# Performance work log

Hardware: AMD Instinct MI355X
Metric: run time of the kernel (lower is better)

The kernel has to match this reference:

```python
import jax, jax.numpy as jnp
import numpy as np
from jax import lax

BN_EPS = 1e-5
DN = ('NCHW', 'OIHW', 'NCHW')


def _bn_silu(y, s, b, m, v):
    # eval-mode BatchNorm2d followed by SiLU
    inv = s / jnp.sqrt(v + BN_EPS)
    y = y * inv[None, :, None, None] + (b - m * inv)[None, :, None, None]
    return jax.nn.silu(y)


def _dsconv(x, dw_w, pw_w, s, b, m, v):
    c = x.shape[1]
    y = lax.conv_general_dilated(x, dw_w, (1, 1), [(1, 1), (1, 1)],
                                 dimension_numbers=DN, feature_group_count=c)
    y = lax.conv_general_dilated(y, pw_w, (1, 1), [(0, 0), (0, 0)],
                                 dimension_numbers=DN)
    return _bn_silu(y, s, b, m, v)


def setup_inputs() -> dict:
    key = jax.random.key(0)
    ks = jax.random.split(key, 8)
    B, C, H, W, OUT, TOPK = 32, 256, 64, 64, 256, 2
    CS = C // 2
    inp = {
        'x': jax.random.normal(ks[0], (B, C, H, W), jnp.float32),
        'weights': jax.random.uniform(ks[1], (B, TOPK), jnp.float32),
        'indices': jax.random.randint(ks[2], (B, TOPK), 0, 4),
        'dw_w0': jax.random.normal(ks[3], (CS, 1, 3, 3), jnp.float32) * 0.1,
        'pw_w0': jax.random.normal(ks[4], (OUT, CS, 1, 1), jnp.float32) * 0.05,
        'bn0_s': jnp.ones((OUT,), jnp.float32),
        'bn0_b': jnp.zeros((OUT,), jnp.float32),
        'bn0_m': jnp.zeros((OUT,), jnp.float32),
        'bn0_v': jnp.ones((OUT,), jnp.float32),
        'dw_w1': jax.random.normal(ks[5], (CS, 1, 3, 3), jnp.float32) * 0.1,
        'pw_w1': jax.random.normal(ks[6], (OUT, CS, 1, 1), jnp.float32) * 0.05,
        'bn1_s': jnp.ones((OUT,), jnp.float32),
        'bn1_b': jnp.zeros((OUT,), jnp.float32),
        'bn1_m': jnp.zeros((OUT,), jnp.float32),
        'bn1_v': jnp.ones((OUT,), jnp.float32),
        'w2': jax.random.normal(ks[7], (OUT, C, 1, 1), jnp.float32) * 0.05,
        'bn2_s': jnp.ones((OUT,), jnp.float32),
        'bn2_b': jnp.zeros((OUT,), jnp.float32),
        'bn2_m': jnp.zeros((OUT,), jnp.float32),
        'bn2_v': jnp.ones((OUT,), jnp.float32),
    }
    return inp


def reference(x, weights, indices,
              dw_w0, pw_w0, bn0_s, bn0_b, bn0_m, bn0_v,
              dw_w1, pw_w1, bn1_s, bn1_b, bn1_m, bn1_v,
              w2, bn2_s, bn2_b, bn2_m, bn2_v):
    cs = x.shape[1] // 2
    x_rgb, x_ir = x[:, :cs], x[:, cs:]
    # Per-expert routing coefficient: sum over top-k slots of weight * (index == e).
    # Mathematically identical to the torch masked scatter-add loop.
    def coeff(e):
        return jnp.sum(weights * (indices == e).astype(weights.dtype), axis=1)  # [B]
    e0 = _dsconv(x_rgb, dw_w0, pw_w0, bn0_s, bn0_b, bn0_m, bn0_v)
    e1 = _dsconv(x_ir, dw_w1, pw_w1, bn1_s, bn1_b, bn1_m, bn1_v)
    e2 = _bn_silu(lax.conv_general_dilated(x, w2, (1, 1), [(0, 0), (0, 0)],
                                           dimension_numbers=DN),
                  bn2_s, bn2_b, bn2_m, bn2_v)
    out = (coeff(0)[:, None, None, None] * e0
           + coeff(1)[:, None, None, None] * e1
           + coeff(2)[:, None, None, None] * e2)
    return out
```

## Files before the change

kernel.cpp:

```cpp
#include <hip/hip_runtime.h>

typedef __bf16 bf16x8 __attribute__((ext_vector_type(8)));
typedef float f32x4 __attribute__((ext_vector_type(4)));

#define BN_EPS 1e-5f

__device__ __forceinline__ unsigned short f2bf(float f) {
    union { float f; unsigned u; } x; x.f = f;
    unsigned r = x.u + 0x7fffu + ((x.u >> 16) & 1u);
    return (unsigned short)(r >> 16);
}

__device__ __forceinline__ unsigned pk_bf16(float lo, float hi) {
    unsigned r;
    asm("v_cvt_pk_bf16_f32 %0, %1, %2" : "=v"(r) : "v"(lo), "v"(hi));
    return r;
}

__device__ __forceinline__ float fcomp(float4 v, int j) {
    return (j == 0) ? v.x : (j == 1) ? v.y : (j == 2) ? v.z : v.w;
}

__global__ void prep_kernel(const float* __restrict__ pw0, const float* __restrict__ pw1,
                            const float* __restrict__ w2,
                            const float* __restrict__ s0, const float* __restrict__ b0,
                            const float* __restrict__ m0, const float* __restrict__ v0,
                            const float* __restrict__ s1, const float* __restrict__ b1,
                            const float* __restrict__ m1, const float* __restrict__ v1,
                            const float* __restrict__ s2, const float* __restrict__ b2,
                            const float* __restrict__ m2, const float* __restrict__ v2,
                            unsigned short* __restrict__ wfF0, unsigned short* __restrict__ wfF1,
                            unsigned short* __restrict__ wfF2, float* __restrict__ beta) {
    int o = blockIdx.x;
    int t = threadIdx.x;
    float inv0 = s0[o] * rsqrtf(v0[o] + BN_EPS);
    float inv1 = s1[o] * rsqrtf(v1[o] + BN_EPS);
    float inv2 = s2[o] * rsqrtf(v2[o] + BN_EPS);
    if (t == 0) {
        beta[0 * 256 + o] = b0[o] - m0[o] * inv0;
        beta[1 * 256 + o] = b1[o] - m1[o] * inv1;
        beta[2 * 256 + o] = b2[o] - m2[o] * inv2;
    }
    if (t < 128) {
        wfF0[((t >> 3) * 256 + o) * 8 + (t & 7)] = f2bf(pw0[o * 128 + t] * inv0);
        wfF1[((t >> 3) * 256 + o) * 8 + (t & 7)] = f2bf(pw1[o * 128 + t] * inv1);
    }
    wfF2[((t >> 3) * 256 + o) * 8 + (t & 7)] = f2bf(w2[o * 256 + t] * inv2);
}

__device__ __forceinline__ void loadA0(const unsigned short* __restrict__ W,
                                       int wave, int l15, int l4, bf16x8 a[2]) {
    const int row0 = wave * 32 + l15;
    a[0] = *(const bf16x8*)(W + (l4 * 256 + row0) * 8);
    a[1] = *(const bf16x8*)(W + (l4 * 256 + row0 + 16) * 8);
}

template<int NK>
__device__ __forceinline__ void gemm_expert(const char* lds, const unsigned short* __restrict__ W,
                                            int qb, int wave, int l15, int l4,
                                            const int* pxv, const int* swv,
                                            const bf16x8 aPre[2], f32x4 acc[2][4]) {
    const int row0 = wave * 32 + l15;
    bf16x8 aC[2], bC[4];
    aC[0] = aPre[0]; aC[1] = aPre[1];
#pragma unroll
    for (int tp = 0; tp < 4; ++tp)
        bC[tp] = *(const bf16x8*)(lds + pxv[tp] * 512 + ((qb + l4 * 16) ^ swv[tp]));

#pragma unroll
    for (int kk = 0; kk < NK; ++kk) {
        bf16x8 aN[2], bN[4];
        if (kk + 1 < NK) {
#pragma unroll
            for (int ot = 0; ot < 2; ++ot)
                aN[ot] = *(const bf16x8*)(W + (((kk + 1) * 4 + l4) * 256 + row0 + ot * 16) * 8);
#pragma unroll
            for (int tp = 0; tp < 4; ++tp)
                bN[tp] = *(const bf16x8*)(lds + pxv[tp] * 512 + ((qb + (kk + 1) * 64 + l4 * 16) ^ swv[tp]));
        }
#pragma unroll
        for (int ot = 0; ot < 2; ++ot)
#pragma unroll
            for (int tp = 0; tp < 4; ++tp)
                acc[ot][tp] = __builtin_amdgcn_mfma_f32_16x16x32_bf16(aC[ot], bC[tp], acc[ot][tp], 0, 0, 0);
        if (kk + 1 < NK) {
#pragma unroll
            for (int ot = 0; ot < 2; ++ot) aC[ot] = aN[ot];
#pragma unroll
            for (int tp = 0; tp < 4; ++tp) bC[tp] = bN[tp];
        }
    }
}

__device__ __forceinline__ void epilogue(const f32x4 acc[2][4], float ce, const float* __restrict__ bp,
                                         int wave, int l4, f32x4 res[2][4]) {
#pragma unroll
    for (int ot = 0; ot < 2; ++ot)
#pragma unroll
        for (int j = 0; j < 4; ++j) {
            const int o = wave * 32 + ot * 16 + l4 * 4 + j;
            const float bet = bp[o];
#pragma unroll
            for (int tp = 0; tp < 4; ++tp) {
                float v = acc[ot][tp][j] + bet;
                float sig = __builtin_amdgcn_rcpf(1.f + __expf(-v));
                res[ot][tp][j] += ce * (v * sig);
            }
        }
}

__global__ __launch_bounds__(512, 4)
void fused_kernel(const float* __restrict__ x,
                  const float* __restrict__ wts, const int* __restrict__ idx,
                  const float* __restrict__ dw0, const float* __restrict__ dw1,
                  const unsigned short* __restrict__ wfF0,
                  const unsigned short* __restrict__ wfF1,
                  const unsigned short* __restrict__ wfF2,
                  const float* __restrict__ beta,
                  float* __restrict__ out) {
    __shared__ __align__(16) char lds[69632];

    const int tid  = threadIdx.x;
    const int wave = tid >> 6;
    const int lane = tid & 63;

    const int bid = blockIdx.x;
    const int xcd = bid & 7;
    const int t8  = bid >> 3;
    const int b   = t8 >> 3;
    const int h   = ((t8 & 7) << 3) | xcd;

    float c0 = 0.f, c1 = 0.f, c2 = 0.f;
#pragma unroll
    for (int t = 0; t < 2; ++t) {
        int e = idx[b * 2 + t];
        float w = wts[b * 2 + t];
        if (e == 0) c0 += w;
        else if (e == 1) c1 += w;
        else if (e == 2) c2 += w;
    }
    const bool do0 = (c0 != 0.f), do1 = (c1 != 0.f), do2 = (c2 != 0.f);

    const long rowBase = (long)b * 1048576L;

    const int g   = lane >> 2;
    const int kq  = lane & 3;
    const int px0 = g * 4;
    const int l15 = lane & 15;
    const int l4  = lane >> 4;
    const float* xb = x + rowBase + h * 64 + px0;
    const bool hm = (h > 0), hp = (h < 63);

    f32x4 res[2][4];
#pragma unroll
    for (int ot = 0; ot < 2; ++ot)
#pragma unroll
        for (int tp = 0; tp < 4; ++tp)
            res[ot][tp] = (f32x4){0.f, 0.f, 0.f, 0.f};

    int pxv[4], swv[4];
#pragma unroll
    for (int tp = 0; tp < 4; ++tp) {
        pxv[tp] = tp * 16 + l15;
        swv[tp] = (pxv[tp] & 15) << 4;
    }

    const bool dwact = (wave < 4) ? do0 : do1;
    if (dwact || do2) {
#pragma unroll
        for (int i = 0; i < 2; ++i) {
            const int k0 = wave * 32 + i * 16 + kq * 4;
            unsigned dw_p[2][4], rw_p[2][4];
#pragma unroll
            for (int pr = 0; pr < 2; ++pr) {
                float y[2][4];
                float4 rcv[2];
#pragma unroll
                for (int k2 = 0; k2 < 2; ++k2) {
                    const int k = k0 + pr * 2 + k2;
                    const float* xc = xb + (long)k * 4096;
                    float4 rc = *(const float4*)(xc);
                    rcv[k2] = rc;
                    if (dwact) {
                        const float* dwp = (k < 128) ? (dw0 + k * 9) : (dw1 + (k - 128) * 9);
                        float4 rm = hm ? *(const float4*)(xc - 64) : make_float4(0.f, 0.f, 0.f, 0.f);
                        float4 rp = hp ? *(const float4*)(xc + 64) : make_float4(0.f, 0.f, 0.f, 0.f);
                        float lm = __shfl_up(rm.w, 4), lc = __shfl_up(rc.w, 4), lp = __shfl_up(rp.w, 4);
                        float Rm = __shfl_down(rm.x, 4), Rc = __shfl_down(rc.x, 4), Rp = __shfl_down(rp.x, 4);
                        if (g == 0)  { lm = 0.f; lc = 0.f; lp = 0.f; }
                        if (g == 15) { Rm = 0.f; Rc = 0.f; Rp = 0.f; }
                        const float w0 = dwp[0], w1 = dwp[1], w2 = dwp[2];
                        const float w3 = dwp[3], w4 = dwp[4], w5 = dwp[5];
                        const float w6 = dwp[6], w7 = dwp[7], w8 = dwp[8];
                        y[k2][0] = w0*lm   + w1*rm.x + w2*rm.y + w3*lc   + w4*rc.x + w5*rc.y + w6*lp   + w7*rp.x + w8*rp.y;
                        y[k2][1] = w0*rm.x + w1*rm.y + w2*rm.z + w3*rc.x + w4*rc.y + w5*rc.z + w6*rp.x + w7*rp.y + w8*rp.z;
                        y[k2][2] = w0*rm.y + w1*rm.z + w2*rm.w + w3*rc.y + w4*rc.z + w5*rc.w + w6*rp.y + w7*rp.z + w8*rp.w;
                        y[k2][3] = w0*rm.z + w1*rm.w + w2*Rm   + w3*rc.z + w4*rc.w + w5*Rc   + w6*rp.z + w7*rp.w + w8*Rp;
                    }
                }
                if (dwact) {
#pragma unroll
                    for (int j = 0; j < 4; ++j)
                        dw_p[pr][j] = pk_bf16(y[0][j], y[1][j]);
                }
                if (do2) {
#pragma unroll
                    for (int j = 0; j < 4; ++j)
                        rw_p[pr][j] = pk_bf16(fcomp(rcv[0], j), fcomp(rcv[1], j));
                }
            }
            const int colb = (k0 >> 3) * 16;
            const int sub  = (k0 & 4) * 2;
#pragma unroll
            for (int j = 0; j < 4; ++j) {
                const int px  = px0 + j;
                const int off = px * 512 + ((colb ^ ((px & 15) << 4))) + sub;
                if (dwact)
                    *(uint2*)(lds + off) = make_uint2(dw_p[0][j], dw_p[1][j]);
                if (do2)
                    *(uint2*)(lds + 32768 + off) = make_uint2(rw_p[0][j], rw_p[1][j]);
            }
        }
    }

    bf16x8 a0[2];
    loadA0(wfF0, wave, l15, l4, a0);

    __syncthreads();

    f32x4 acc[2][4];
    if (do0) {
#pragma unroll
        for (int ot = 0; ot < 2; ++ot)
#pragma unroll
            for (int tp = 0; tp < 4; ++tp) acc[ot][tp] = (f32x4){0.f, 0.f, 0.f, 0.f};
        gemm_expert<4>(lds, wfF0, 0, wave, l15, l4, pxv, swv, a0, acc);
    }
    bf16x8 a1[2];
    loadA0(wfF1, wave, l15, l4, a1);
    if (do0) epilogue(acc, c0, beta, wave, l4, res);

    if (do1) {
#pragma unroll
        for (int ot = 0; ot < 2; ++ot)
#pragma unroll
            for (int tp = 0; tp < 4; ++tp) acc[ot][tp] = (f32x4){0.f, 0.f, 0.f, 0.f};
        gemm_expert<4>(lds, wfF1, 256, wave, l15, l4, pxv, swv, a1, acc);
    }
    bf16x8 a2[2];
    loadA0(wfF2, wave, l15, l4, a2);
    if (do1) epilogue(acc, c1, beta + 256, wave, l4, res);

    if (do2) {
#pragma unroll
        for (int ot = 0; ot < 2; ++ot)
#pragma unroll
            for (int tp = 0; tp < 4; ++tp) acc[ot][tp] = (f32x4){0.f, 0.f, 0.f, 0.f};
        gemm_expert<8>(lds + 32768, wfF2, 0, wave, l15, l4, pxv, swv, a2, acc);
        epilogue(acc, c2, beta + 512, wave, l4, res);
    }

    float* lf = (float*)lds;
    const long outB = rowBase + h * 64;
    __syncthreads();
    {
        const int reg  = wave >> 2;
        const int rbase = reg * 8704;
#pragma unroll
        for (int ot = 0; ot < 2; ++ot)
#pragma unroll
            for (int j = 0; j < 4; ++j) {
                const int row = (wave & 3) * 32 + ot * 16 + l4 * 4 + j;
#pragma unroll
                for (int tp = 0; tp < 4; ++tp)
                    lf[rbase + row * 68 + tp * 16 + l15] = res[ot][tp][j];
            }
    }
    __syncthreads();
    {
        const int rowq = tid >> 3;
        const int col  = (tid & 7) * 8;
#pragma unroll
        for (int rr = 0; rr < 4; ++rr) {
            const int lr = rowq + rr * 64;
            const int ad = (lr >> 7) * 8704 + (lr & 127) * 68 + col;
            float4 v0 = *(float4*)&lf[ad];
            float4 v1 = *(float4*)&lf[ad + 4];
            float* op = out + outB + (long)lr * 4096 + col;
            *(float4*)op = v0;
            *(float4*)(op + 4) = v1;
        }
    }
}

extern "C" void kernel_launch(void* const* d_in, const int* in_sizes, int n_in,
                              void* d_out, int out_size, void* d_ws, size_t ws_size,
                              hipStream_t stream) {
    const float* x    = (const float*)d_in[0];
    const float* wts  = (const float*)d_in[1];
    const int*   idx  = (const int*)d_in[2];
    const float* dw0  = (const float*)d_in[3];
    const float* pw0  = (const float*)d_in[4];
    const float* s0   = (const float*)d_in[5];
    const float* b0   = (const float*)d_in[6];
    const float* m0   = (const float*)d_in[7];
    const float* v0   = (const float*)d_in[8];
    const float* dw1  = (const float*)d_in[9];
    const float* pw1  = (const float*)d_in[10];
    const float* s1   = (const float*)d_in[11];
    const float* b1   = (const float*)d_in[12];
    const float* m1   = (const float*)d_in[13];
    const float* v1   = (const float*)d_in[14];
    const float* w2   = (const float*)d_in[15];
    const float* s2   = (const float*)d_in[16];
    const float* b2   = (const float*)d_in[17];
    const float* m2   = (const float*)d_in[18];
    const float* v2   = (const float*)d_in[19];

    char* ws = (char*)d_ws;
    unsigned short* wfF0 = (unsigned short*)ws;
    unsigned short* wfF1 = (unsigned short*)(ws + 65536);
    unsigned short* wfF2 = (unsigned short*)(ws + 131072);
    float*          beta = (float*)(ws + 262144);

    prep_kernel<<<256, 256, 0, stream>>>(pw0, pw1, w2,
                                         s0, b0, m0, v0,
                                         s1, b1, m1, v1,
                                         s2, b2, m2, v2,
                                         wfF0, wfF1, wfF2, beta);

    fused_kernel<<<2048, 512, 0, stream>>>(x, wts, idx, dw0, dw1,
                                           wfF0, wfF1, wfF2, beta, (float*)d_out);
}
```

Baseline: 95.21 us.

## Software-pipeline depthwise staging loads, cache dw weights in LDS, remap block order

Restructures the input staging loop into four stages, each prefetching the next pair of channel rows into registers while computing the current depthwise conv and writing packed bf16 to LDS. The depthwise weights are preloaded into a padded LDS table, so per-channel weight fetches come from LDS rather than global memory. The block-to-(batch,row) mapping also changes so that each XCD handles a contiguous range of rows. The cost is a larger LDS footprint (80KB), which may reduce occupancy, plus higher register pressure from the prefetch buffers and an extra barrier.

```diff
diff --git a/kernel.cpp b/kernel.cpp
--- a/kernel.cpp
+++ b/kernel.cpp
@@ -118,17 +118,16 @@
                   const unsigned short* __restrict__ wfF2,
                   const float* __restrict__ beta,
                   float* __restrict__ out) {
-    __shared__ __align__(16) char lds[69632];
+    __shared__ __align__(16) char lds[81920];
 
     const int tid  = threadIdx.x;
     const int wave = tid >> 6;
     const int lane = tid & 63;
 
     const int bid = blockIdx.x;
-    const int xcd = bid & 7;
-    const int t8  = bid >> 3;
-    const int b   = t8 >> 3;
-    const int h   = ((t8 & 7) << 3) | xcd;
+    const int nb  = ((bid & 7) << 8) | (bid >> 3);
+    const int b   = nb >> 6;
+    const int h   = nb & 63;
 
     float c0 = 0.f, c1 = 0.f, c2 = 0.f;
 #pragma unroll
@@ -165,60 +164,104 @@
         swv[tp] = (pxv[tp] & 15) << 4;
     }
 
+    float* ldw = (float*)(lds + 69632);
+    if (do0 || do1) {
+#pragma unroll
+        for (int r = 0; r < 6; ++r) {
+            const int t  = tid + r * 512;
+            const int ch = t / 12;
+            const int c9 = t - ch * 12;
+            float v = 0.f;
+            if (c9 < 9) v = (ch < 128) ? dw0[ch * 9 + c9] : dw1[(ch - 128) * 9 + c9];
+            ldw[t] = v;
+        }
+    }
+
     const bool dwact = (wave < 4) ? do0 : do1;
-    if (dwact || do2) {
-#pragma unroll
-        for (int i = 0; i < 2; ++i) {
-            const int k0 = wave * 32 + i * 16 + kq * 4;
-            unsigned dw_p[2][4], rw_p[2][4];
-#pragma unroll
-            for (int pr = 0; pr < 2; ++pr) {
-                float y[2][4];
-                float4 rcv[2];
-#pragma unroll
-                for (int k2 = 0; k2 < 2; ++k2) {
-                    const int k = k0 + pr * 2 + k2;
-                    const float* xc = xb + (long)k * 4096;
-                    float4 rc = *(const float4*)(xc);
-                    rcv[k2] = rc;
-                    if (dwact) {
-                        const float* dwp = (k < 128) ? (dw0 + k * 9) : (dw1 + (k - 128) * 9);
-                        float4 rm = hm ? *(const float4*)(xc - 64) : make_float4(0.f, 0.f, 0.f, 0.f);
-                        float4 rp = hp ? *(const float4*)(xc + 64) : make_float4(0.f, 0.f, 0.f, 0.f);
-                        float lm = __shfl_up(rm.w, 4), lc = __shfl_up(rc.w, 4), lp = __shfl_up(rp.w, 4);
-                        float Rm = __shfl_down(rm.x, 4), Rc = __shfl_down(rc.x, 4), Rp = __shfl_down(rp.x, 4);
-                        if (g == 0)  { lm = 0.f; lc = 0.f; lp = 0.f; }
-                        if (g == 15) { Rm = 0.f; Rc = 0.f; Rp = 0.f; }
-                        const float w0 = dwp[0], w1 = dwp[1], w2 = dwp[2];
-                        const float w3 = dwp[3], w4 = dwp[4], w5 = dwp[5];
-                        const float w6 = dwp[6], w7 = dwp[7], w8 = dwp[8];
-                        y[k2][0] = w0*lm   + w1*rm.x + w2*rm.y + w3*lc   + w4*rc.x + w5*rc.y + w6*lp   + w7*rp.x + w8*rp.y;
-                        y[k2][1] = w0*rm.x + w1*rm.y + w2*rm.z + w3*rc.x + w4*rc.y + w5*rc.z + w6*rp.x + w7*rp.y + w8*rp.z;
-                        y[k2][2] = w0*rm.y + w1*rm.z + w2*rm.w + w3*rc.y + w4*rc.z + w5*rc.w + w6*rp.y + w7*rp.z + w8*rp.w;
-                        y[k2][3] = w0*rm.z + w1*rm.w + w2*Rm   + w3*rc.z + w4*rc.w + w5*Rc   + w6*rp.z + w7*rp.w + w8*Rp;
-                    }
+    const bool stg = dwact || do2;
+    const float4 z4 = make_float4(0.f, 0.f, 0.f, 0.f);
+
+    float4 cm0, cc0, cp0, cm1, cc1, cp1;
+    float4 nm0, nc0, np0, nm1, nc1, np1;
+    if (stg) {
+        const int k = wave * 32 + kq * 4;
+        const float* x0 = xb + (long)k * 4096;
+        const float* x1 = x0 + 4096;
+        cc0 = *(const float4*)x0;
+        cc1 = *(const float4*)x1;
+        cm0 = (dwact && hm) ? *(const float4*)(x0 - 64) : z4;
+        cp0 = (dwact && hp) ? *(const float4*)(x0 + 64) : z4;
+        cm1 = (dwact && hm) ? *(const float4*)(x1 - 64) : z4;
+        cp1 = (dwact && hp) ? *(const float4*)(x1 + 64) : z4;
+    }
+    __syncthreads();
+
+    if (stg) {
+#pragma unroll
+        for (int p = 0; p < 4; ++p) {
+            const int k = wave * 32 + ((p >> 1) << 4) + kq * 4 + ((p & 1) << 1);
+            if (p < 3) {
+                const int pn = p + 1;
+                const int kn = wave * 32 + ((pn >> 1) << 4) + kq * 4 + ((pn & 1) << 1);
+                const float* x0 = xb + (long)kn * 4096;
+                const float* x1 = x0 + 4096;
+                nc0 = *(const float4*)x0;
+                nc1 = *(const float4*)x1;
+                nm0 = (dwact && hm) ? *(const float4*)(x0 - 64) : z4;
+                np0 = (dwact && hp) ? *(const float4*)(x0 + 64) : z4;
+                nm1 = (dwact && hm) ? *(const float4*)(x1 - 64) : z4;
+                np1 = (dwact && hp) ? *(const float4*)(x1 + 64) : z4;
+            }
+            const int colb = (k >> 3) * 16;
+            const int sub  = (k & 7) * 2;
+            if (dwact) {
+                float y0[4], y1[4];
+                {
+                    const float* wp = ldw + k * 12;
+                    const float w0 = wp[0], w1 = wp[1], w2 = wp[2];
+                    const float w3 = wp[3], w4 = wp[4], w5 = wp[5];
+                    const float w6 = wp[6], w7 = wp[7], w8 = wp[8];
+                    float lm = __shfl_up(cm0.w, 4), lc = __shfl_up(cc0.w, 4), lp = __shfl_up(cp0.w, 4);
+                    float Rm = __shfl_down(cm0.x, 4), Rc = __shfl_down(cc0.x, 4), Rp = __shfl_down(cp0.x, 4);
+                    if (g == 0)  { lm = 0.f; lc = 0.f; lp = 0.f; }
+                    if (g == 15) { Rm = 0.f; Rc = 0.f; Rp = 0.f; }
+                    y0[0] = w0*lm    + w1*cm0.x + w2*cm0.y + w3*lc    + w4*cc0.x + w5*cc0.y + w6*lp    + w7*cp0.x + w8*cp0.y;
+                    y0[1] = w0*cm0.x + w1*cm0.y + w2*cm0.z + w3*cc0.x + w4*cc0.y + w5*cc0.z + w6*cp0.x + w7*cp0.y + w8*cp0.z;
+                    y0[2] = w0*cm0.y + w1*cm0.z + w2*cm0.w + w3*cc0.y + w4*cc0.z + w5*cc0.w + w6*cp0.y + w7*cp0.z + w8*cp0.w;
+                    y0[3] = w0*cm0.z + w1*cm0.w + w2*Rm    + w3*cc0.z + w4*cc0.w + w5*Rc    + w6*cp0.z + w7*cp0.w + w8*Rp;
                 }
-                if (dwact) {
-#pragma unroll
-                    for (int j = 0; j < 4; ++j)
-                        dw_p[pr][j] = pk_bf16(y[0][j], y[1][j]);
+                {
+                    const float* wp = ldw + (k + 1) * 12;
+                    const float w0 = wp[0], w1 = wp[1], w2 = wp[2];
+                    const float w3 = wp[3], w4 = wp[4], w5 = wp[5];
+                    const float w6 = wp[6], w7 = wp[7], w8 = wp[8];
+                    float lm = __shfl_up(cm1.w, 4), lc = __shfl_up(cc1.w, 4), lp = __shfl_up(cp1.w, 4);
+                    float Rm = __shfl_down(cm1.x, 4), Rc = __shfl_down(cc1.x, 4), Rp = __shfl_down(cp1.x, 4);
+                    if (g == 0)  { lm = 0.f; lc = 0.f; lp = 0.f; }
+                    if (g == 15) { Rm = 0.f; Rc = 0.f; Rp = 0.f; }
+                    y1[0] = w0*lm    + w1*cm1.x + w2*cm1.y + w3*lc    + w4*cc1.x + w5*cc1.y + w6*lp    + w7*cp1.x + w8*cp1.y;
+                    y1[1] = w0*cm1.x + w1*cm1.y + w2*cm1.z + w3*cc1.x + w4*cc1.y + w5*cc1.z + w6*cp1.x + w7*cp1.y + w8*cp1.z;
+                    y1[2] = w0*cm1.y + w1*cm1.z + w2*cm1.w + w3*cc1.y + w4*cc1.z + w5*cc1.w + w6*cp1.y + w7*cp1.z + w8*cp1.w;
+                    y1[3] = w0*cm1.z + w1*cm1.w + w2*Rm    + w3*cc1.z + w4*cc1.w + w5*Rc    + w6*cp1.z + w7*cp1.w + w8*Rp;
                 }
-                if (do2) {
-#pragma unroll
-                    for (int j = 0; j < 4; ++j)
-                        rw_p[pr][j] = pk_bf16(fcomp(rcv[0], j), fcomp(rcv[1], j));
+#pragma unroll
+                for (int j = 0; j < 4; ++j) {
+                    const int px = px0 + j;
+                    *(unsigned*)(lds + px * 512 + ((colb ^ ((px & 15) << 4))) + sub) =
+                        pk_bf16(y0[j], y1[j]);
                 }
             }
-            const int colb = (k0 >> 3) * 16;
-            const int sub  = (k0 & 4) * 2;
-#pragma unroll
-            for (int j = 0; j < 4; ++j) {
-                const int px  = px0 + j;
-                const int off = px * 512 + ((colb ^ ((px & 15) << 4))) + sub;
-                if (dwact)
-                    *(uint2*)(lds + off) = make_uint2(dw_p[0][j], dw_p[1][j]);
-                if (do2)
-                    *(uint2*)(lds + 32768 + off) = make_uint2(rw_p[0][j], rw_p[1][j]);
+            if (do2) {
+#pragma unroll
+                for (int j = 0; j < 4; ++j) {
+                    const int px = px0 + j;
+                    *(unsigned*)(lds + 32768 + px * 512 + ((colb ^ ((px & 15) << 4))) + sub) =
+                        pk_bf16(fcomp(cc0, j), fcomp(cc1, j));
+                }
+            }
+            if (p < 3) {
+                cm0 = nm0; cc0 = nc0; cp0 = np0;
+                cm1 = nm1; cc1 = nc1; cp1 = np1;
             }
         }
     }
@@ -264,7 +307,7 @@
     const long outB = rowBase + h * 64;
     __syncthreads();
     {
-        const int reg  = wave >> 2;
+        const int reg   = wave >> 2;
         const int rbase = reg * 8704;
 #pragma unroll
         for (int ot = 0; ot < 2; ++ot)
```

Result: slower. 102.2 us (+7.3%).

## Split each image row into two 32-pixel half-row tiles per block

Applied to the files above, without the earlier changes.

Each block now handles a half row of 32 pixels instead of a full 64-pixel row, doubling the grid to 4096 blocks. This halves the LDS footprint and the per-wave accumulator and register count, which should allow more resident blocks and better latency hiding. The depthwise halo at the tile edges is now fetched with extra scalar loads, and the block index is remapped for XCD locality. In exchange, each A-fragment of weights is reused across fewer pixels per MFMA, so weight loads are amortized over less work, and the halo loads are duplicated.

```diff
diff --git a/kernel.cpp b/kernel.cpp
--- a/kernel.cpp
+++ b/kernel.cpp
@@ -59,41 +59,41 @@
 __device__ __forceinline__ void gemm_expert(const char* lds, const unsigned short* __restrict__ W,
                                             int qb, int wave, int l15, int l4,
                                             const int* pxv, const int* swv,
-                                            const bf16x8 aPre[2], f32x4 acc[2][4]) {
+                                            const bf16x8 aPre[2], f32x4 acc[2][2]) {
     const int row0 = wave * 32 + l15;
-    bf16x8 aC[2], bC[4];
+    bf16x8 aC[2], bC[2];
     aC[0] = aPre[0]; aC[1] = aPre[1];
 #pragma unroll
-    for (int tp = 0; tp < 4; ++tp)
+    for (int tp = 0; tp < 2; ++tp)
         bC[tp] = *(const bf16x8*)(lds + pxv[tp] * 512 + ((qb + l4 * 16) ^ swv[tp]));
 
 #pragma unroll
     for (int kk = 0; kk < NK; ++kk) {
-        bf16x8 aN[2], bN[4];
+        bf16x8 aN[2], bN[2];
         if (kk + 1 < NK) {
 #pragma unroll
             for (int ot = 0; ot < 2; ++ot)
                 aN[ot] = *(const bf16x8*)(W + (((kk + 1) * 4 + l4) * 256 + row0 + ot * 16) * 8);
 #pragma unroll
-            for (int tp = 0; tp < 4; ++tp)
+            for (int tp = 0; tp < 2; ++tp)
                 bN[tp] = *(const bf16x8*)(lds + pxv[tp] * 512 + ((qb + (kk + 1) * 64 + l4 * 16) ^ swv[tp]));
         }
 #pragma unroll
         for (int ot = 0; ot < 2; ++ot)
 #pragma unroll
-            for (int tp = 0; tp < 4; ++tp)
+            for (int tp = 0; tp < 2; ++tp)
                 acc[ot][tp] = __builtin_amdgcn_mfma_f32_16x16x32_bf16(aC[ot], bC[tp], acc[ot][tp], 0, 0, 0);
         if (kk + 1 < NK) {
 #pragma unroll
             for (int ot = 0; ot < 2; ++ot) aC[ot] = aN[ot];
 #pragma unroll
-            for (int tp = 0; tp < 4; ++tp) bC[tp] = bN[tp];
-        }
-    }
-}
-
-__device__ __forceinline__ void epilogue(const f32x4 acc[2][4], float ce, const float* __restrict__ bp,
-                                         int wave, int l4, f32x4 res[2][4]) {
+            for (int tp = 0; tp < 2; ++tp) bC[tp] = bN[tp];
+        }
+    }
+}
+
+__device__ __forceinline__ void epilogue(const f32x4 acc[2][2], float ce, const float* __restrict__ bp,
+                                         int wave, int l4, f32x4 res[2][2]) {
 #pragma unroll
     for (int ot = 0; ot < 2; ++ot)
 #pragma unroll
@@ -101,7 +101,7 @@
             const int o = wave * 32 + ot * 16 + l4 * 4 + j;
             const float bet = bp[o];
 #pragma unroll
-            for (int tp = 0; tp < 4; ++tp) {
+            for (int tp = 0; tp < 2; ++tp) {
                 float v = acc[ot][tp][j] + bet;
                 float sig = __builtin_amdgcn_rcpf(1.f + __expf(-v));
                 res[ot][tp][j] += ce * (v * sig);
@@ -118,17 +118,18 @@
                   const unsigned short* __restrict__ wfF2,
                   const float* __restrict__ beta,
                   float* __restrict__ out) {
-    __shared__ __align__(16) char lds[69632];
+    __shared__ __align__(16) char lds[36864];
 
     const int tid  = threadIdx.x;
     const int wave = tid >> 6;
     const int lane = tid & 63;
 
     const int bid = blockIdx.x;
-    const int xcd = bid & 7;
-    const int t8  = bid >> 3;
-    const int b   = t8 >> 3;
-    const int h   = ((t8 & 7) << 3) | xcd;
+    const int nb  = ((bid & 7) << 9) | (bid >> 3);
+    const int whalf = nb & 1;
+    const int h     = (nb >> 1) & 63;
+    const int b     = nb >> 7;
+    const int wlo   = whalf * 32;
 
     float c0 = 0.f, c1 = 0.f, c2 = 0.f;
 #pragma unroll
@@ -143,82 +144,89 @@
 
     const long rowBase = (long)b * 1048576L;
 
-    const int g   = lane >> 2;
-    const int kq  = lane & 3;
+    const int g   = lane >> 3;
+    const int kq  = lane & 7;
     const int px0 = g * 4;
     const int l15 = lane & 15;
     const int l4  = lane >> 4;
-    const float* xb = x + rowBase + h * 64 + px0;
+    const float* xr = x + rowBase + h * 64;
     const bool hm = (h > 0), hp = (h < 63);
-
-    f32x4 res[2][4];
+    const bool wl_ok = (whalf == 1);
+    const bool wr_ok = (whalf == 0);
+
+    f32x4 res[2][2];
 #pragma unroll
     for (int ot = 0; ot < 2; ++ot)
 #pragma unroll
-        for (int tp = 0; tp < 4; ++tp)
+        for (int tp = 0; tp < 2; ++tp)
             res[ot][tp] = (f32x4){0.f, 0.f, 0.f, 0.f};
 
-    int pxv[4], swv[4];
-#pragma unroll
-    for (int tp = 0; tp < 4; ++tp) {
+    int pxv[2], swv[2];
+#pragma unroll
+    for (int tp = 0; tp < 2; ++tp) {
         pxv[tp] = tp * 16 + l15;
         swv[tp] = (pxv[tp] & 15) << 4;
     }
 
     const bool dwact = (wave < 4) ? do0 : do1;
-    if (dwact || do2) {
-#pragma unroll
-        for (int i = 0; i < 2; ++i) {
-            const int k0 = wave * 32 + i * 16 + kq * 4;
-            unsigned dw_p[2][4], rw_p[2][4];
-#pragma unroll
-            for (int pr = 0; pr < 2; ++pr) {
-                float y[2][4];
-                float4 rcv[2];
-#pragma unroll
-                for (int k2 = 0; k2 < 2; ++k2) {
-                    const int k = k0 + pr * 2 + k2;
-                    const float* xc = xb + (long)k * 4096;
-                    float4 rc = *(const float4*)(xc);
-                    rcv[k2] = rc;
-                    if (dwact) {
-                        const float* dwp = (k < 128) ? (dw0 + k * 9) : (dw1 + (k - 128) * 9);
-                        float4 rm = hm ? *(const float4*)(xc - 64) : make_float4(0.f, 0.f, 0.f, 0.f);
-                        float4 rp = hp ? *(const float4*)(xc + 64) : make_float4(0.f, 0.f, 0.f, 0.f);
-                        float lm = __shfl_up(rm.w, 4), lc = __shfl_up(rc.w, 4), lp = __shfl_up(rp.w, 4);
-                        float Rm = __shfl_down(rm.x, 4), Rc = __shfl_down(rc.x, 4), Rp = __shfl_down(rp.x, 4);
-                        if (g == 0)  { lm = 0.f; lc = 0.f; lp = 0.f; }
-                        if (g == 15) { Rm = 0.f; Rc = 0.f; Rp = 0.f; }
-                        const float w0 = dwp[0], w1 = dwp[1], w2 = dwp[2];
-                        const float w3 = dwp[3], w4 = dwp[4], w5 = dwp[5];
-                        const float w6 = dwp[6], w7 = dwp[7], w8 = dwp[8];
-                        y[k2][0] = w0*lm   + w1*rm.x + w2*rm.y + w3*lc   + w4*rc.x + w5*rc.y + w6*lp   + w7*rp.x + w8*rp.y;
-                        y[k2][1] = w0*rm.x + w1*rm.y + w2*rm.z + w3*rc.x + w4*rc.y + w5*rc.z + w6*rp.x + w7*rp.y + w8*rp.z;
-                        y[k2][2] = w0*rm.y + w1*rm.z + w2*rm.w + w3*rc.y + w4*rc.z + w5*rc.w + w6*rp.y + w7*rp.z + w8*rp.w;
-                        y[k2][3] = w0*rm.z + w1*rm.w + w2*Rm   + w3*rc.z + w4*rc.w + w5*Rc   + w6*rp.z + w7*rp.w + w8*Rp;
-                    }
-                }
+    const bool stg = dwact || do2;
+    const float4 z4 = make_float4(0.f, 0.f, 0.f, 0.f);
+
+    float4 mR[2][2], cR[2][2], pR[2][2];
+    float lx[2][2][3], rx[2][2][3];
+    if (stg) {
+#pragma unroll
+        for (int pp = 0; pp < 2; ++pp) {
+#pragma unroll
+            for (int q = 0; q < 2; ++q) {
+                const int k = wave * 32 + pp * 16 + kq * 2 + q;
+                const float* base = xr + (long)k * 4096 + wlo + px0;
+                cR[pp][q] = *(const float4*)base;
                 if (dwact) {
-#pragma unroll
-                    for (int j = 0; j < 4; ++j)
-                        dw_p[pr][j] = pk_bf16(y[0][j], y[1][j]);
-                }
-                if (do2) {
-#pragma unroll
-                    for (int j = 0; j < 4; ++j)
-                        rw_p[pr][j] = pk_bf16(fcomp(rcv[0], j), fcomp(rcv[1], j));
+                    mR[pp][q] = hm ? *(const float4*)(base - 64) : z4;
+                    pR[pp][q] = hp ? *(const float4*)(base + 64) : z4;
+                    lx[pp][q][0] = (g == 0 && wl_ok && hm) ? xr[(long)k * 4096 - 64 + wlo - 1] : 0.f;
+                    lx[pp][q][1] = (g == 0 && wl_ok)       ? xr[(long)k * 4096 + wlo - 1]       : 0.f;
+                    lx[pp][q][2] = (g == 0 && wl_ok && hp) ? xr[(long)k * 4096 + 64 + wlo - 1]  : 0.f;
+                    rx[pp][q][0] = (g == 7 && wr_ok && hm) ? xr[(long)k * 4096 - 64 + wlo + 32] : 0.f;
+                    rx[pp][q][1] = (g == 7 && wr_ok)       ? xr[(long)k * 4096 + wlo + 32]      : 0.f;
+                    rx[pp][q][2] = (g == 7 && wr_ok && hp) ? xr[(long)k * 4096 + 64 + wlo + 32] : 0.f;
                 }
             }
-            const int colb = (k0 >> 3) * 16;
-            const int sub  = (k0 & 4) * 2;
+        }
+#pragma unroll
+        for (int pp = 0; pp < 2; ++pp) {
+            const int kA = wave * 32 + pp * 16 + kq * 2;
+            float y[2][4];
+            if (dwact) {
+#pragma unroll
+                for (int q = 0; q < 2; ++q) {
+                    const int k = kA + q;
+                    const float* dwp = (k < 128) ? (dw0 + k * 9) : (dw1 + (k - 128) * 9);
+                    float4 m = mR[pp][q], c = cR[pp][q], p = pR[pp][q];
+                    float lm = __shfl_up(m.w, 8), lc = __shfl_up(c.w, 8), lp = __shfl_up(p.w, 8);
+                    float Rm = __shfl_down(m.x, 8), Rc = __shfl_down(c.x, 8), Rp = __shfl_down(p.x, 8);
+                    if (g == 0) { lm = lx[pp][q][0]; lc = lx[pp][q][1]; lp = lx[pp][q][2]; }
+                    if (g == 7) { Rm = rx[pp][q][0]; Rc = rx[pp][q][1]; Rp = rx[pp][q][2]; }
+                    const float w0 = dwp[0], w1 = dwp[1], w2 = dwp[2];
+                    const float w3 = dwp[3], w4 = dwp[4], w5 = dwp[5];
+                    const float w6 = dwp[6], w7 = dwp[7], w8 = dwp[8];
+                    y[q][0] = w0*lm  + w1*m.x + w2*m.y + w3*lc  + w4*c.x + w5*c.y + w6*lp  + w7*p.x + w8*p.y;
+                    y[q][1] = w0*m.x + w1*m.y + w2*m.z + w3*c.x + w4*c.y + w5*c.z + w6*p.x + w7*p.y + w8*p.z;
+                    y[q][2] = w0*m.y + w1*m.z + w2*m.w + w3*c.y + w4*c.z + w5*c.w + w6*p.y + w7*p.z + w8*p.w;
+                    y[q][3] = w0*m.z + w1*m.w + w2*Rm  + w3*c.z + w4*c.w + w5*Rc  + w6*p.z + w7*p.w + w8*Rp;
+                }
+            }
+            const int colb = (kA >> 3) * 16;
+            const int sub  = (kA & 7) * 2;
 #pragma unroll
             for (int j = 0; j < 4; ++j) {
                 const int px  = px0 + j;
                 const int off = px * 512 + ((colb ^ ((px & 15) << 4))) + sub;
                 if (dwact)
-                    *(uint2*)(lds + off) = make_uint2(dw_p[0][j], dw_p[1][j]);
+                    *(unsigned*)(lds + off) = pk_bf16(y[0][j], y[1][j]);
                 if (do2)
-                    *(uint2*)(lds + 32768 + off) = make_uint2(rw_p[0][j], rw_p[1][j]);
+                    *(unsigned*)(lds + 16384 + off) = pk_bf16(fcomp(cR[pp][0], j), fcomp(cR[pp][1], j));
             }
         }
     }
@@ -228,12 +236,12 @@
 
     __syncthreads();
 
-    f32x4 acc[2][4];
+    f32x4 acc[2][2];
     if (do0) {
 #pragma unroll
         for (int ot = 0; ot < 2; ++ot)
 #pragma unroll
-            for (int tp = 0; tp < 4; ++tp) acc[ot][tp] = (f32x4){0.f, 0.f, 0.f, 0.f};
+            for (int tp = 0; tp < 2; ++tp) acc[ot][tp] = (f32x4){0.f, 0.f, 0.f, 0.f};
         gemm_expert<4>(lds, wfF0, 0, wave, l15, l4, pxv, swv, a0, acc);
     }
     bf16x8 a1[2];
@@ -244,7 +252,7 @@
 #pragma unroll
         for (int ot = 0; ot < 2; ++ot)
 #pragma unroll
-            for (int tp = 0; tp < 4; ++tp) acc[ot][tp] = (f32x4){0.f, 0.f, 0.f, 0.f};
+            for (int tp = 0; tp < 2; ++tp) acc[ot][tp] = (f32x4){0.f, 0.f, 0.f, 0.f};
         gemm_expert<4>(lds, wfF1, 256, wave, l15, l4, pxv, swv, a1, acc);
     }
     bf16x8 a2[2];
@@ -255,40 +263,32 @@
 #pragma unroll
         for (int ot = 0; ot < 2; ++ot)
 #pragma unroll
-            for (int tp = 0; tp < 4; ++tp) acc[ot][tp] = (f32x4){0.f, 0.f, 0.f, 0.f};
-        gemm_expert<8>(lds + 32768, wfF2, 0, wave, l15, l4, pxv, swv, a2, acc);
+            for (int tp = 0; tp < 2; ++tp) acc[ot][tp] = (f32x4){0.f, 0.f, 0.f, 0.f};
+        gemm_expert<8>(lds + 16384, wfF2, 0, wave, l15, l4, pxv, swv, a2, acc);
         epilogue(acc, c2, beta + 512, wave, l4, res);
     }
 
     float* lf = (float*)lds;
-    const long outB = rowBase + h * 64;
+    const long outB = rowBase + h * 64 + wlo;
+    __syncthreads();
+#pragma unroll
+    for (int ot = 0; ot < 2; ++ot)
+#pragma unroll
+        for (int j = 0; j < 4; ++j) {
+            const int o = wave * 32 + ot * 16 + l4 * 4 + j;
+#pragma unroll
+            for (int tp = 0; tp < 2; ++tp)
+                lf[o * 36 + tp * 16 + l15] = res[ot][tp][j];
+        }
     __syncthreads();
     {
-        const int reg  = wave >> 2;
-        const int rbase = reg * 8704;
-#pragma unroll
-        for (int ot = 0; ot < 2; ++ot)
-#pragma unroll
-            for (int j = 0; j < 4; ++j) {
-                const int row = (wave & 3) * 32 + ot * 16 + l4 * 4 + j;
-#pragma unroll
-                for (int tp = 0; tp < 4; ++tp)
-                    lf[rbase + row * 68 + tp * 16 + l15] = res[ot][tp][j];
-            }
-    }
-    __syncthreads();
-    {
-        const int rowq = tid >> 3;
-        const int col  = (tid & 7) * 8;
-#pragma unroll
-        for (int rr = 0; rr < 4; ++rr) {
-            const int lr = rowq + rr * 64;
-            const int ad = (lr >> 7) * 8704 + (lr & 127) * 68 + col;
-            float4 v0 = *(float4*)&lf[ad];
-            float4 v1 = *(float4*)&lf[ad + 4];
-            float* op = out + outB + (long)lr * 4096 + col;
-            *(float4*)op = v0;
-            *(float4*)(op + 4) = v1;
+        const int row = tid >> 1;
+        const int col = (tid & 1) * 16;
+        float* op = out + outB + (long)row * 4096 + col;
+#pragma unroll
+        for (int cc = 0; cc < 4; ++cc) {
+            float4 v = *(float4*)&lf[row * 36 + col + cc * 4];
+            *(float4*)(op + cc * 4) = v;
         }
     }
 }
@@ -329,6 +329,6 @@
                                          s2, b2, m2, v2,
                                          wfF0, wfF1, wfF2, beta);
 
-    fused_kernel<<<2048, 512, 0, stream>>>(x, wts, idx, dw0, dw1,
+    fused_kernel<<<4096, 512, 0, stream>>>(x, wts, idx, dw0, dw1,
                                            wfF0, wfF1, wfF2, beta, (float*)d_out);
 }
```

Result: slower. 128.0 us (+34.4%).
